# Kernel optimization log

Hardware: AMD Instinct MI355X
Metric: run time of the kernel (lower is better)

## Reference

```python
import jax, jax.numpy as jnp
import numpy as np

B, T, D, H = 4, 2048, 1024, 16
DK, DV, K, I = 48, 96, 4, 3072
EPS = 1e-5


def rmsnorm(x, w, eps=EPS):
    return x * jax.lax.rsqrt(jnp.mean(x * x, -1, keepdims=True) + eps) * w


def l2norm(x, eps=1e-6):
    return x * jax.lax.rsqrt(jnp.sum(x * x, -1, keepdims=True) + eps)


def causal_conv(x, w):
    # x: [B,T,C], w: [C,K]; causal depthwise conv (torch cross-correlation semantics)
    k = w.shape[1]
    xp = jnp.pad(x, ((0, 0), (k - 1, 0), (0, 0))).transpose(0, 2, 1)  # [B,C,T+K-1]
    y = jax.lax.conv_general_dilated(xp, w[:, None, :], (1,), 'VALID',
                                     feature_group_count=w.shape[0])
    return y.transpose(0, 2, 1)


def gated_delta_rule(q, k, v, g, beta):
    # q,k: [B,T,H,DK]  v: [B,T,H,DV]  g,beta: [B,T,H]
    scale = q.shape[-1] ** -0.5
    qT = jnp.moveaxis(q, 1, 0) * scale
    kT = jnp.moveaxis(k, 1, 0)
    vT = jnp.moveaxis(v, 1, 0)
    gT = jnp.moveaxis(g, 1, 0)
    bT = jnp.moveaxis(beta, 1, 0)
    S0 = jnp.zeros((q.shape[0], q.shape[2], q.shape[3], v.shape[3]), q.dtype)

    def step(S, inp):
        q_t, k_t, v_t, g_t, b_t = inp
        S = S * jnp.exp(g_t)[..., None, None]                      # gated decay
        v_new = (v_t - jnp.einsum('bhk,bhkv->bhv', k_t, S)) * b_t[..., None]
        S = S + k_t[..., None] * v_new[..., None, :]               # delta-rule update
        o_t = jnp.einsum('bhk,bhkv->bhv', q_t, S)
        return S, o_t

    _, o = jax.lax.scan(step, S0, (qT, kT, vT, gT, bT))
    return jnp.moveaxis(o, 0, 1)


def setup_inputs() -> dict:
    key = jax.random.key(0)
    ks = jax.random.split(key, 20)
    s = 0.02
    return {
        'hidden_states': jax.random.normal(ks[0], (B, T, D), jnp.float32),
        'norm1_w': jnp.ones((D,), jnp.float32),
        'q_w': jax.random.normal(ks[1], (D, H * DK), jnp.float32) * s,
        'k_w': jax.random.normal(ks[2], (D, H * DK), jnp.float32) * s,
        'v_w': jax.random.normal(ks[3], (D, H * DV), jnp.float32) * s,
        'conv_q_w': jax.random.normal(ks[4], (H * DK, K), jnp.float32) * 0.2,
        'conv_k_w': jax.random.normal(ks[5], (H * DK, K), jnp.float32) * 0.2,
        'conv_v_w': jax.random.normal(ks[6], (H * DV, K), jnp.float32) * 0.2,
        'b_w': jax.random.normal(ks[7], (D, H), jnp.float32) * s,
        'a_w': jax.random.normal(ks[8], (D, H), jnp.float32) * s,
        'A_log': jnp.log(jax.random.uniform(ks[9], (H,), jnp.float32, 1.0, 16.0)),
        'dt_bias': jax.random.normal(ks[10], (H,), jnp.float32) * 0.5,
        'g_w': jax.random.normal(ks[11], (D, H * DV), jnp.float32) * s,
        'o_norm_w': jnp.ones((DV,), jnp.float32),
        'o_w': jax.random.normal(ks[12], (H * DV, D), jnp.float32) * s,
        'norm2_w': jnp.ones((D,), jnp.float32),
        'gate_w': jax.random.normal(ks[13], (D, I), jnp.float32) * s,
        'up_w': jax.random.normal(ks[14], (D, I), jnp.float32) * s,
        'down_w': jax.random.normal(ks[15], (I, D), jnp.float32) * s,
    }


def reference(hidden_states, norm1_w, q_w, k_w, v_w, conv_q_w, conv_k_w, conv_v_w,
              b_w, a_w, A_log, dt_bias, g_w, o_norm_w, o_w, norm2_w,
              gate_w, up_w, down_w):
    x = hidden_states
    h = rmsnorm(x, norm1_w)
    # --- GatedDeltaNet mixer ---
    q = jax.nn.silu(causal_conv(h @ q_w, conv_q_w)).reshape(B, T, H, DK)
    k = jax.nn.silu(causal_conv(h @ k_w, conv_k_w)).reshape(B, T, H, DK)
    v = jax.nn.silu(causal_conv(h @ v_w, conv_v_w)).reshape(B, T, H, DV)
    q, k = l2norm(q), l2norm(k)
    beta = jax.nn.sigmoid(h @ b_w)                                  # [B,T,H]
    g = -jnp.exp(A_log) * jax.nn.softplus(h @ a_w + dt_bias)        # [B,T,H] mamba gate
    o = gated_delta_rule(q, k, v, g, beta)                          # [B,T,H,DV]
    gate = (h @ g_w).reshape(B, T, H, DV)
    o = rmsnorm(o, o_norm_w) * (gate * jax.nn.sigmoid(gate))        # fused gated RMSNorm
    x = x + o.reshape(B, T, H * DV) @ o_w
    # --- SwiGLU MLP ---
    h2 = rmsnorm(x, norm2_w)
    x = x + (jax.nn.silu(h2 @ gate_w) * (h2 @ up_w)) @ down_w
    return x
```

## Files before the change

kernel.cpp:

```cpp
#include <hip/hip_runtime.h>
#include <hip/hip_bf16.h>
#include <math.h>

constexpr int Bn = 4, Tn = 2048, Dn = 1024, Hn = 16, DKn = 48, DVn = 96, In = 3072;
constexpr int BT = Bn * Tn;
constexpr int HDK = Hn * DKn;
constexpr int HDV = Hn * DVn;
constexpr int QKVC = 2 * HDK + HDV;
constexpr int CC = 64;
constexpr int NC = Tn / CC;

using bf16 = __hip_bfloat16;
typedef __attribute__((ext_vector_type(8))) short bf16x8;
typedef __attribute__((ext_vector_type(4))) float f32x4;

constexpr size_t WO_HBF   = 0;
constexpr size_t WO_QKVR  = 16777216;
constexpr size_t WO_OSC   = 16777216;
constexpr size_t WO_ACT   = 16777216;
constexpr size_t WO_A     = 16777216;
constexpr size_t WO_B     = 26214400;
constexpr size_t WO_ST    = 45088768;
constexpr size_t WO_QKVC  = 67108864;
constexpr size_t WO_GATE  = 117440512;
constexpr size_t WO_X1    = 142606336;
constexpr size_t WO_BA    = 176160768;
constexpr size_t WO_GC    = 177209344;
constexpr size_t WO_T     = 177733632;
constexpr size_t WO_UV    = 194510848;
constexpr size_t WO_WB    = 219676672;
constexpr size_t WB_QKVT = 0;
constexpr size_t WB_GT   = 3145728;
constexpr size_t WB_OT   = 4718592;
constexpr size_t WB_GATET= 6291456;
constexpr size_t WB_UPT  = 9437184;
constexpr size_t WB_DOWNT= 12582912;
constexpr size_t WB_ABT  = 15728640;

__device__ __forceinline__ float sigmoidf_(float x) { return 1.f / (1.f + __expf(-x)); }
__device__ __forceinline__ float siluf(float x) { return x * sigmoidf_(x); }

__device__ __forceinline__ void glds16(const void* g, void* l) {
  __builtin_amdgcn_global_load_lds((const __attribute__((address_space(1))) void*)g,
                                   (__attribute__((address_space(3))) void*)l, 16, 0, 0);
}

__device__ __forceinline__ f32x4 mfma16(bf16x8 a, bf16x8 b, f32x4 c) {
  return __builtin_amdgcn_mfma_f32_16x16x32_bf16(a, b, c, 0, 0, 0);
}

__device__ __forceinline__ bf16x8 scale8(bf16x8 a, float s) {
  bf16x8 r;
#pragma unroll
  for (int e = 0; e < 8; e++) {
    float f = __bfloat162float(__ushort_as_bfloat16((unsigned short)a[e])) * s;
    r[e] = (short)__bfloat16_as_ushort(__float2bfloat16(f));
  }
  return r;
}

__device__ __forceinline__ float b2f(short u) {
  return __bfloat162float(__ushort_as_bfloat16((unsigned short)u));
}
__device__ __forceinline__ short f2b(float f) {
  return (short)__bfloat16_as_ushort(__float2bfloat16(f));
}

struct TcastArgs {
  const float* src[10];
  bf16* dst[10];
  int R[10], C[10], gxw[10], t0[10];
};

__global__ void tcast_all(TcastArgs a) {
  __shared__ float t[32][33];
  int bid = blockIdx.x;
  int i = 0;
#pragma unroll
  for (int k = 1; k < 10; k++) if (bid >= a.t0[k]) i = k;
  int lt = bid - a.t0[i];
  int gxw = a.gxw[i];
  int bx = lt % gxw, by = lt / gxw;
  const float* in = a.src[i];
  bf16* out = a.dst[i];
  int R = a.R[i], C = a.C[i];
  int tx = threadIdx.x, ty = threadIdx.y;
  int c0 = bx * 32, r0 = by * 32;
#pragma unroll
  for (int j = 0; j < 4; j++) {
    int r = ty + j * 8;
    float v = (c0 + tx < C) ? in[(size_t)(r0 + r) * C + c0 + tx] : 0.f;
    t[r][tx] = v;
  }
  __syncthreads();
#pragma unroll
  for (int j = 0; j < 4; j++) {
    int cc = ty + j * 8;
    if (c0 + cc < C) out[(size_t)(c0 + cc) * R + r0 + tx] = __float2bfloat16(t[tx][cc]);
  }
}

__global__ void rmsnorm_bf_k(const float* __restrict__ x, const float* __restrict__ w,
                             bf16* __restrict__ y) {
  int row = blockIdx.x;
  const float4* xr = (const float4*)(x + (size_t)row * Dn);
  int tid = threadIdx.x;
  float4 v = xr[tid];
  float ss = v.x * v.x + v.y * v.y + v.z * v.z + v.w * v.w;
  for (int m = 32; m >= 1; m >>= 1) ss += __shfl_xor(ss, m, 64);
  __shared__ float wsum[4];
  if ((tid & 63) == 0) wsum[tid >> 6] = ss;
  __syncthreads();
  ss = wsum[0] + wsum[1] + wsum[2] + wsum[3];
  float rs = rsqrtf(ss * (1.f / Dn) + 1e-5f);
  float4 wv = ((const float4*)w)[tid];
  bf16* yr = y + (size_t)row * Dn + tid * 4;
  yr[0] = __float2bfloat16(v.x * rs * wv.x);
  yr[1] = __float2bfloat16(v.y * rs * wv.y);
  yr[2] = __float2bfloat16(v.z * rs * wv.z);
  yr[3] = __float2bfloat16(v.w * rs * wv.w);
}

#define AS256(bi) (lds + (bi) * 8192)
#define BS256(bi) (lds + 32768 + (bi) * 8192)
#define STAGE256(bi, k0) do { \
    glds16(gA0 + (k0), AS256(bi) + w * 512); \
    glds16(gB0 + (k0), BS256(bi) + w * 512); \
  } while (0)

__global__ __launch_bounds__(1024) void gemm256(
    const bf16* __restrict__ A, const bf16* __restrict__ Bt,
    bf16* __restrict__ C0, bf16* __restrict__ C1,
    int gx, int N, int K, int mode) {
  __shared__ bf16 lds[65536];
  int nb = gx * 32;
  int q8 = nb >> 3;
  int bid = blockIdx.x;
  int sw = (bid & 7) * q8 + (bid >> 3);
  int by = sw & 31, bx = sw >> 5;
  int bm = by * 256, bn = bx * 256;
  int tid = threadIdx.x;
  int lane = tid & 63, w = tid >> 6;
  int l15 = lane & 15, lq = lane >> 4;
  int wr = w >> 2, wc = w & 3;
  int arow0 = tid >> 2;
  int srcq = (tid & 3) ^ ((arow0 >> 1) & 3);
  const bf16* gA0 = A + (size_t)(bm + arow0) * K + srcq * 8;
  const bf16* gB0 = Bt + (size_t)(bn + arow0) * K + srcq * 8;
  int slot = lq ^ ((l15 >> 1) & 3);
  f32x4 acc[4][4];
#pragma unroll
  for (int m = 0; m < 4; m++)
#pragma unroll
    for (int n = 0; n < 4; n++) acc[m][n] = (f32x4){0.f, 0.f, 0.f, 0.f};
  int NT = K >> 5;
  STAGE256(0, 0);
  STAGE256(1, 32);
  STAGE256(2, 64);
  for (int t = 0; t < NT; ++t) {
    int b = t & 3;
    if (t <= NT - 3)      { asm volatile("s_waitcnt vmcnt(4)" ::: "memory"); }
    else if (t == NT - 2) { asm volatile("s_waitcnt vmcnt(2)" ::: "memory"); }
    else                  { asm volatile("s_waitcnt vmcnt(0)" ::: "memory"); }
    __builtin_amdgcn_s_barrier();
    bf16x8 af[4], bfr[4];
#pragma unroll
    for (int m = 0; m < 4; m++)
      af[m] = *(const bf16x8*)(AS256(b) + (wr * 64 + m * 16 + l15) * 32 + slot * 8);
#pragma unroll
    for (int n = 0; n < 4; n++)
      bfr[n] = *(const bf16x8*)(BS256(b) + (wc * 64 + n * 16 + l15) * 32 + slot * 8);
    __builtin_amdgcn_s_setprio(1);
#pragma unroll
    for (int m = 0; m < 4; m++)
#pragma unroll
      for (int n = 0; n < 4; n++)
        acc[m][n] = mfma16(af[m], bfr[n], acc[m][n]);
    __builtin_amdgcn_s_setprio(0);
    if (t + 3 < NT) STAGE256((t + 3) & 3, (t + 3) * 32);
  }
  __syncthreads();
  bf16* dst; int ldc, bnl; bool doSilu;
  if (mode == 10) {
    if (bn < 3072) { dst = C0; ldc = 3072; bnl = bn; doSilu = false; }
    else           { dst = C1; ldc = 1536; bnl = bn - 3072; doSilu = false; }
  } else {
    if (bn < 3072) { dst = C0; ldc = 3072; bnl = bn; doSilu = true; }
    else           { dst = C1; ldc = 3072; bnl = bn - 3072; doSilu = false; }
  }
  bf16* cw = lds + w * 4096;
#pragma unroll
  for (int m = 0; m < 4; m++)
#pragma unroll
    for (int n = 0; n < 4; n++)
#pragma unroll
      for (int i = 0; i < 4; i++) {
        int row_l = m * 16 + lq * 4 + i;
        int col_l = n * 16 + l15;
        float v = acc[m][n][i];
        if (doSilu) v = siluf(v);
        cw[row_l * 64 + (col_l ^ ((row_l & 7) << 3))] = __float2bfloat16(v);
      }
  __syncthreads();
  int r8 = lane >> 3, cblk = lane & 7;
#pragma unroll
  for (int it = 0; it < 8; it++) {
    int row_l = it * 8 + r8;
    int sblk = cblk ^ (row_l & 7);
    bf16x8 val = *(const bf16x8*)&cw[row_l * 64 + sblk * 8];
    *(bf16x8*)&dst[(size_t)(bm + wr * 64 + row_l) * ldc + bnl + wc * 64 + cblk * 8] = val;
  }
}

__global__ __launch_bounds__(1024) void gemm_mfma(
    const bf16* __restrict__ A, const bf16* __restrict__ Bt,
    void* __restrict__ Cv, const float* __restrict__ res,
    int N, int K, int ldc, int mode) {
  __shared__ bf16 As[4][4096];
  __shared__ bf16 Bs[4][4096];
  int tid = threadIdx.x, lane = tid & 63, w = tid >> 6;
  int bm = blockIdx.y * 128, bn = blockIdx.x * 128;
  int l15 = lane & 15, lq = lane >> 4;
  int wr = w >> 2, wc = w & 3;
  int r0 = (tid & 511) >> 2;
  int sq = (tid & 3) ^ ((r0 >> 1) & 3);
  const bf16* g0;
  bf16* lb;
  if (w < 8) {
    g0 = A + (size_t)(bm + r0) * K + sq * 8;
    lb = &As[0][w * 512];
  } else {
    int br = bn + r0; if (br >= N) br = 0;
    g0 = Bt + (size_t)br * K + sq * 8;
    lb = &Bs[0][(w - 8) * 512];
  }
#define STAGE128X(bi, k0) glds16(g0 + (k0), lb + (bi) * 4096)
  int slot = lq ^ ((l15 >> 1) & 3);
  f32x4 acc[2][2];
#pragma unroll
  for (int m = 0; m < 2; m++)
#pragma unroll
    for (int n = 0; n < 2; n++) acc[m][n] = (f32x4){0.f, 0.f, 0.f, 0.f};
  int NT = K >> 5;
  STAGE128X(0, 0);
  STAGE128X(1, 32);
  STAGE128X(2, 64);
  for (int t = 0; t < NT; ++t) {
    int b = t & 3;
    if (t <= NT - 3)      { asm volatile("s_waitcnt vmcnt(2)" ::: "memory"); }
    else if (t == NT - 2) { asm volatile("s_waitcnt vmcnt(1)" ::: "memory"); }
    else                  { asm volatile("s_waitcnt vmcnt(0)" ::: "memory"); }
    __builtin_amdgcn_s_barrier();
    bf16x8 af[2], bfr[2];
#pragma unroll
    for (int m = 0; m < 2; m++)
      af[m] = *(const bf16x8*)&As[b][(wr * 32 + m * 16 + l15) * 32 + slot * 8];
#pragma unroll
    for (int n = 0; n < 2; n++)
      bfr[n] = *(const bf16x8*)&Bs[b][(wc * 32 + n * 16 + l15) * 32 + slot * 8];
    __builtin_amdgcn_s_setprio(1);
#pragma unroll
    for (int m = 0; m < 2; m++)
#pragma unroll
      for (int n = 0; n < 2; n++)
        acc[m][n] = mfma16(af[m], bfr[n], acc[m][n]);
    __builtin_amdgcn_s_setprio(0);
    if (t + 3 < NT) STAGE128X((t + 3) & 3, (t + 3) * 32);
  }
#pragma unroll
  for (int m = 0; m < 2; m++) {
#pragma unroll
    for (int n = 0; n < 2; n++) {
      int col = bn + wc * 32 + n * 16 + l15;
      if (col >= N) continue;
#pragma unroll
      for (int i = 0; i < 4; i++) {
        int row = bm + wr * 32 + m * 16 + lq * 4 + i;
        float v = acc[m][n][i];
        size_t idx = (size_t)row * ldc + col;
        if (mode == 0) {
          if (res) v += res[idx];
          ((float*)Cv)[idx] = v;
        } else {
          ((bf16*)Cv)[idx] = __float2bfloat16(v);
        }
      }
    }
  }
}

__global__ __launch_bounds__(256) void convsilu2_k(const bf16* __restrict__ in,
                                                   bf16* __restrict__ outp,
                                                   const float* __restrict__ wq,
                                                   const float* __restrict__ wk,
                                                   const float* __restrict__ wv) {
  int tx = threadIdx.x & 31;
  int ty = threadIdx.x >> 5;
  int c = (blockIdx.x * 32 + tx) * 8;
  int gt = blockIdx.y * 8 + ty;
  int b = gt >> 11, t = gt & (Tn - 1);
  const float* wsrc = (c < HDK) ? (wq + c * 4)
                     : (c < 2 * HDK) ? (wk + (c - HDK) * 4)
                                     : (wv + (c - 2 * HDK) * 4);
  float4 W[8];
#pragma unroll
  for (int j = 0; j < 8; j++) W[j] = ((const float4*)wsrc)[j];
  const bf16* base = in + (size_t)b * Tn * QKVC + c;
  bf16x8 r[4];
  bf16x8 zero = {0, 0, 0, 0, 0, 0, 0, 0};
#pragma unroll
  for (int j = 0; j < 4; j++) {
    int tt = t - 3 + j;
    r[j] = (tt >= 0) ? *(const bf16x8*)(base + (size_t)tt * QKVC) : zero;
  }
  bf16x8 o;
#pragma unroll
  for (int ch = 0; ch < 8; ch++) {
    float x0 = b2f(r[0][ch]), x1 = b2f(r[1][ch]), x2 = b2f(r[2][ch]), x3 = b2f(r[3][ch]);
    float y = x0 * W[ch].x + x1 * W[ch].y + x2 * W[ch].z + x3 * W[ch].w;
    o[ch] = f2b(siluf(y));
  }
  *(bf16x8*)(outp + (size_t)gt * QKVC + c) = o;
}

__global__ __launch_bounds__(256) void l2norm_k(bf16* __restrict__ qkv) {
  int row = blockIdx.x * 256 + threadIdx.x;
  int t = row >> 5, hr = row & 31;
  bf16* p = qkv + (size_t)t * QKVC + hr * DKn;
  bf16x8 v[6];
  float ss = 0.f;
#pragma unroll
  for (int j = 0; j < 6; j++) {
    v[j] = *(const bf16x8*)(p + j * 8);
#pragma unroll
    for (int e = 0; e < 8; e++) { float f = b2f(v[j][e]); ss += f * f; }
  }
  float rs = rsqrtf(ss + 1e-6f);
#pragma unroll
  for (int j = 0; j < 6; j++) {
    bf16x8 o;
#pragma unroll
    for (int e = 0; e < 8; e++) o[e] = f2b(b2f(v[j][e]) * rs);
    *(bf16x8*)(p + j * 8) = o;
  }
}

__global__ void betag_k(float* __restrict__ ba, const float* __restrict__ A_log,
                        const float* __restrict__ dt_bias) {
  int i = blockIdx.x * blockDim.x + threadIdx.x;
  int h = i & 15, r = i >> 4;
  float bv = ba[(size_t)r * 32 + h];
  float av = ba[(size_t)r * 32 + 16 + h];
  ba[(size_t)r * 32 + h] = sigmoidf_(bv);
  float xx = av + dt_bias[h];
  float sp = (xx > 20.f) ? xx : log1pf(__expf(xx));
  ba[(size_t)r * 32 + 16 + h] = -__expf(A_log[h]) * sp;
}

__global__ __launch_bounds__(256) void dn_p1a(const bf16* __restrict__ qkv,
                                              const float* __restrict__ ba,
                                              float* __restrict__ Gc_g,
                                              bf16* __restrict__ T_g,
                                              bf16* __restrict__ Uv_g,
                                              bf16* __restrict__ A_g,
                                              bf16* __restrict__ B_g) {
  __shared__ __align__(16) char smem[62976];
  bf16 (*Kl)[72]   = (bf16(*)[72])(smem);
  bf16 (*Tl)[72]   = (bf16(*)[72])(smem + 9216);
  bf16 (*UvdT)[72] = (bf16(*)[72])(smem + 18432);
  float* Gcl = (float*)(smem + 32256);
  float* Bl  = (float*)(smem + 32512);
  bf16 (*Vl)[100]  = (bf16(*)[100])(smem + 32768);
  float (*Nl)[68]  = (float(*)[68])(smem + 45568);
  bf16 (*KTl)[72]  = (bf16(*)[72])(smem + 32768);
  bf16 (*KTbl)[72] = (bf16(*)[72])(smem + 39680);
  bf16 (*M2T)[72]  = (bf16(*)[72])(smem + 46592);
  int cid = blockIdx.x;
  int nc = cid & (NC - 1);
  int bh = cid >> 5;
  int h = bh & 15, b = bh >> 4;
  int t0 = nc * CC;
  int tid = threadIdx.x, lane = tid & 63, w = tid >> 6;
  int l15 = lane & 15, qd = lane >> 4;
  bf16 zb = __float2bfloat16(0.f);
  {
    int t = tid >> 2, p = tid & 3;
    const bf16* row = qkv + ((size_t)(b * Tn + t0 + t)) * QKVC;
    int c0 = p * 12;
#pragma unroll
    for (int j = 0; j < 12; ++j) Kl[t][c0 + j] = row[HDK + h * DKn + c0 + j];
    int j0 = p * 24;
#pragma unroll
    for (int j = 0; j < 24; ++j) Vl[t][j0 + j] = row[2 * HDK + h * DVn + j0 + j];
  }
  for (int i = tid; i < 64 * 24; i += 256) {
    int t = i / 24, c = 48 + (i % 24);
    Kl[t][c] = zb;
  }
  if (tid < 64) {
    size_t row = (size_t)(b * Tn + t0 + tid);
    float g = ba[row * 32 + 16 + h];
    float be = ba[row * 32 + h];
    float acc = g;
#pragma unroll
    for (int d = 1; d < 64; d <<= 1) {
      float o = __shfl_up(acc, d);
      if (tid >= d) acc += o;
    }
    Gcl[tid] = acc; Bl[tid] = be;
    Gc_g[(size_t)bh * Tn + t0 + tid] = acc;
  }
  __syncthreads();
  f32x4 dacc[4];
#pragma unroll
  for (int n = 0; n < 4; n++) dacc[n] = (f32x4){0.f, 0.f, 0.f, 0.f};
  {
    int arow = w * 16 + l15;
    bf16x8 a0 = *(const bf16x8*)&Kl[arow][qd * 8];
    bf16x8 a1 = *(const bf16x8*)&Kl[arow][32 + qd * 8];
#pragma unroll
    for (int n = 0; n < 4; n++) {
      int brow = n * 16 + l15;
      bf16x8 b0 = *(const bf16x8*)&Kl[brow][qd * 8];
      bf16x8 b1 = *(const bf16x8*)&Kl[brow][32 + qd * 8];
      dacc[n] = mfma16(a0, b0, dacc[n]);
      dacc[n] = mfma16(a1, b1, dacc[n]);
    }
  }
#pragma unroll
  for (int i = 0; i < 4; i++) {
    int t = w * 16 + qd * 4 + i;
    float bt = Bl[t], gt = Gcl[t];
#pragma unroll
    for (int n = 0; n < 4; n++) {
      int s = n * 16 + l15;
      Nl[t][s] = (s < t) ? bt * __expf(gt - Gcl[s]) * dacc[n][i] : 0.f;
    }
  }
  __syncthreads();
  float g63 = Gcl[63];
  int c = tid;
  if (c < 160) {
    float R[64];
    if (c < 64) {
#pragma unroll
      for (int t = 0; t < 64; ++t) R[t] = (t == c) ? 1.f : 0.f;
    } else {
      int j = c - 64;
#pragma unroll
      for (int t = 0; t < 64; ++t) R[t] = Bl[t] * __bfloat162float(Vl[t][j]);
    }
#pragma unroll
    for (int t = 1; t < 64; ++t) {
      float a0 = 0.f, a1 = 0.f, a2 = 0.f, a3 = 0.f;
#pragma unroll
      for (int s = 0; s + 3 < t; s += 4) {
        float4 n4 = *(const float4*)&Nl[t][s];
        a0 += n4.x * R[s]; a1 += n4.y * R[s + 1];
        a2 += n4.z * R[s + 2]; a3 += n4.w * R[s + 3];
      }
#pragma unroll
      for (int s = t & ~3; s < t; ++s) a0 += Nl[t][s] * R[s];
      R[t] -= ((a0 + a1) + (a2 + a3));
    }
    if (c < 64) {
#pragma unroll
      for (int t = 0; t < 64; ++t) {
        bf16 v = __float2bfloat16(R[t]);
        T_g[(size_t)cid * 4096 + t * 64 + c] = v;
        Tl[t][c] = v;
      }
    } else {
      int j = c - 64;
#pragma unroll
      for (int t = 0; t < 64; ++t) {
        Uv_g[(size_t)cid * 6144 + t * 96 + j] = __float2bfloat16(R[t]);
        UvdT[j][t] = __float2bfloat16(R[t] * __expf(g63 - Gcl[t]));
      }
    }
  }
  __syncthreads();
  for (int i = tid; i < 48 * 64; i += 256) {
    int dk = i >> 6, t = i & 63;
    bf16 kv = Kl[t][dk];
    KTl[dk][t] = kv;
    float bl = Bl[t] * __expf(Gcl[t]);
    KTbl[dk][t] = __float2bfloat16(__bfloat162float(kv) * bl);
  }
  __syncthreads();
  f32x4 m1[3];
#pragma unroll
  for (int n = 0; n < 3; n++) m1[n] = (f32x4){0.f, 0.f, 0.f, 0.f};
  {
    int arow = w * 16 + l15;
    bf16x8 a0 = *(const bf16x8*)&Tl[arow][qd * 8];
    bf16x8 a1 = *(const bf16x8*)&Tl[arow][32 + qd * 8];
#pragma unroll
    for (int n = 0; n < 3; n++) {
      int brow = n * 16 + l15;
      bf16x8 b0 = *(const bf16x8*)&KTbl[brow][qd * 8];
      bf16x8 b1 = *(const bf16x8*)&KTbl[brow][32 + qd * 8];
      m1[n] = mfma16(a0, b0, m1[n]);
      m1[n] = mfma16(a1, b1, m1[n]);
    }
  }
#pragma unroll
  for (int i = 0; i < 4; i++) {
    int tt = w * 16 + qd * 4 + i;
    float dd = __expf(g63 - Gcl[tt]);
#pragma unroll
    for (int n = 0; n < 3; n++) {
      int dk = n * 16 + l15;
      M2T[dk][tt] = __float2bfloat16(m1[n][i] * dd);
    }
  }
  __syncthreads();
  float lamC = __expf(g63);
#pragma unroll
  for (int tswap = 0; tswap < 7; tswap++) {
    int t = w + 4 * tswap;
    if (t >= 27) break;
    int mi, ni; bool isA;
    if (t < 9) { isA = true; mi = t / 3; ni = t % 3; }
    else { isA = false; mi = (t - 9) / 6; ni = (t - 9) % 6; }
    f32x4 acc = (f32x4){0.f, 0.f, 0.f, 0.f};
    int arow = mi * 16 + l15;
    bf16x8 a0 = *(const bf16x8*)&KTl[arow][qd * 8];
    bf16x8 a1 = *(const bf16x8*)&KTl[arow][32 + qd * 8];
    int brow = ni * 16 + l15;
    if (isA) {
      bf16x8 b0 = *(const bf16x8*)&M2T[brow][qd * 8];
      bf16x8 b1 = *(const bf16x8*)&M2T[brow][32 + qd * 8];
      acc = mfma16(a0, b0, acc);
      acc = mfma16(a1, b1, acc);
#pragma unroll
      for (int i = 0; i < 4; i++) {
        int row = mi * 16 + qd * 4 + i, colv = ni * 16 + l15;
        float v = ((row == colv) ? lamC : 0.f) - acc[i];
        A_g[(size_t)cid * 2304 + row * 48 + colv] = __float2bfloat16(v);
      }
    } else {
      bf16x8 b0 = *(const bf16x8*)&UvdT[brow][qd * 8];
      bf16x8 b1 = *(const bf16x8*)&UvdT[brow][32 + qd * 8];
      acc = mfma16(a0, b0, acc);
      acc = mfma16(a1, b1, acc);
#pragma unroll
      for (int i = 0; i < 4; i++) {
        int row = mi * 16 + qd * 4 + i, colv = ni * 16 + l15;
        B_g[(size_t)cid * 4608 + row * 96 + colv] = __float2bfloat16(acc[i]);
      }
    }
  }
}

__global__ __launch_bounds__(256) void dn_p2b(const bf16* __restrict__ A_g,
                                              const bf16* __restrict__ B_g,
                                              bf16* __restrict__ St_g) {
  __shared__ bf16 STl[2][96][72];
  __shared__ bf16 Al[2][48][72];
  __shared__ bf16 Bl[2][4608];
  int bh = blockIdx.x;
  int tid = threadIdx.x, lane = tid & 63, w = tid >> 6;
  int l15 = lane & 15, qd = lane >> 4;
  bf16 zb = __float2bfloat16(0.f);
  for (int i = tid; i < 2 * 96 * 72; i += 256) (&STl[0][0][0])[i] = zb;
  for (int i = tid; i < 2 * 48 * 24; i += 256) {
    int buf = i / (48 * 24), r = (i / 24) % 48, cc = 48 + (i % 24);
    Al[buf][r][cc] = zb;
  }
  bf16x8 ra0, ra1, rb0, rb1;
  unsigned int rb2;
  int e_a0 = tid * 8, e_a1 = 2048 + tid * 8;
  {
    size_t cid = (size_t)bh * NC;
    ra0 = *(const bf16x8*)(A_g + cid * 2304 + e_a0);
    if (tid < 32) ra1 = *(const bf16x8*)(A_g + cid * 2304 + e_a1);
    rb0 = *(const bf16x8*)(B_g + cid * 4608 + tid * 16);
    rb1 = *(const bf16x8*)(B_g + cid * 4608 + tid * 16 + 8);
    rb2 = *(const unsigned int*)(B_g + cid * 4608 + 4096 + tid * 2);
  }
  *(bf16x8*)&Al[0][e_a0 / 48][e_a0 % 48] = ra0;
  if (tid < 32) *(bf16x8*)&Al[0][e_a1 / 48][e_a1 % 48] = ra1;
  *(bf16x8*)&Bl[0][tid * 16] = rb0;
  *(bf16x8*)&Bl[0][tid * 16 + 8] = rb1;
  *(unsigned int*)&Bl[0][4096 + tid * 2] = rb2;
  {
    size_t cid = (size_t)bh * NC + 1;
    ra0 = *(const bf16x8*)(A_g + cid * 2304 + e_a0);
    if (tid < 32) ra1 = *(const bf16x8*)(A_g + cid * 2304 + e_a1);
    rb0 = *(const bf16x8*)(B_g + cid * 4608 + tid * 16);
    rb1 = *(const bf16x8*)(B_g + cid * 4608 + tid * 16 + 8);
    rb2 = *(const unsigned int*)(B_g + cid * 4608 + 4096 + tid * 2);
  }
  __syncthreads();

  for (int c = 0; c < NC - 1; ++c) {
    int cur = c & 1, nxt = cur ^ 1;
    size_t cid = (size_t)bh * NC + c;
    {
      int e0 = tid * 8, e1 = 2048 + tid * 8, e2 = 4096 + tid * 2;
      *(bf16x8*)(St_g + cid * 4608 + e0) = *(const bf16x8*)&STl[cur][e0 / 48][e0 % 48];
      *(bf16x8*)(St_g + cid * 4608 + e1) = *(const bf16x8*)&STl[cur][e1 / 48][e1 % 48];
      *(unsigned int*)(St_g + cid * 4608 + e2) = *(const unsigned int*)&STl[cur][e2 / 48][e2 % 48];
    }
    float vals[5][4];
#pragma unroll
    for (int ts = 0; ts < 5; ts++) {
      int t = w + 4 * ts;
      if (t >= 18) break;
      int mi = t / 3, ni = t % 3;
      f32x4 acc = (f32x4){0.f, 0.f, 0.f, 0.f};
      int arow = mi * 16 + l15;
      bf16x8 a0 = *(const bf16x8*)&STl[cur][arow][qd * 8];
      bf16x8 a1 = *(const bf16x8*)&STl[cur][arow][32 + qd * 8];
      int brow = ni * 16 + l15;
      bf16x8 b0 = *(const bf16x8*)&Al[cur][brow][qd * 8];
      bf16x8 b1 = *(const bf16x8*)&Al[cur][brow][32 + qd * 8];
      acc = mfma16(a0, b0, acc);
      acc = mfma16(a1, b1, acc);
#pragma unroll
      for (int i = 0; i < 4; i++) {
        int dv = mi * 16 + qd * 4 + i, ii = ni * 16 + l15;
        vals[ts][i] = acc[i] + __bfloat162float(Bl[cur][ii * 96 + dv]);
      }
    }
#pragma unroll
    for (int ts = 0; ts < 5; ts++) {
      int t = w + 4 * ts;
      if (t >= 18) break;
      int mi = t / 3, ni = t % 3;
#pragma unroll
      for (int i = 0; i < 4; i++) {
        int dv = mi * 16 + qd * 4 + i, ii = ni * 16 + l15;
        STl[nxt][dv][ii] = __float2bfloat16(vals[ts][i]);
      }
    }
    if (c + 1 <= NC - 2) {
      *(bf16x8*)&Al[nxt][e_a0 / 48][e_a0 % 48] = ra0;
      if (tid < 32) *(bf16x8*)&Al[nxt][e_a1 / 48][e_a1 % 48] = ra1;
      *(bf16x8*)&Bl[nxt][tid * 16] = rb0;
      *(bf16x8*)&Bl[nxt][tid * 16 + 8] = rb1;
      *(unsigned int*)&Bl[nxt][4096 + tid * 2] = rb2;
      if (c + 2 <= NC - 2) {
        size_t cid2 = (size_t)bh * NC + c + 2;
        ra0 = *(const bf16x8*)(A_g + cid2 * 2304 + e_a0);
        if (tid < 32) ra1 = *(const bf16x8*)(A_g + cid2 * 2304 + e_a1);
        rb0 = *(const bf16x8*)(B_g + cid2 * 4608 + tid * 16);
        rb1 = *(const bf16x8*)(B_g + cid2 * 4608 + tid * 16 + 8);
        rb2 = *(const unsigned int*)(B_g + cid2 * 4608 + 4096 + tid * 2);
      }
    }
    __syncthreads();
  }
  {
    size_t cid = (size_t)bh * NC + (NC - 1);
    int cur = (NC - 1) & 1;
    int e0 = tid * 8, e1 = 2048 + tid * 8, e2 = 4096 + tid * 2;
    *(bf16x8*)(St_g + cid * 4608 + e0) = *(const bf16x8*)&STl[cur][e0 / 48][e0 % 48];
    *(bf16x8*)(St_g + cid * 4608 + e1) = *(const bf16x8*)&STl[cur][e1 / 48][e1 % 48];
    *(unsigned int*)(St_g + cid * 4608 + e2) = *(const unsigned int*)&STl[cur][e2 / 48][e2 % 48];
  }
}

__global__ __launch_bounds__(256) void dn_p2c(const bf16* __restrict__ qkv,
                                              const float* __restrict__ ba,
                                              const float* __restrict__ Gc_g,
                                              const bf16* __restrict__ T_g,
                                              const bf16* __restrict__ Uv_g,
                                              const bf16* __restrict__ St_g,
                                              const bf16* __restrict__ gate,
                                              const float* __restrict__ onw,
                                              bf16* __restrict__ attn) {
  __shared__ bf16 Kl[64][72], Ql[64][72], Tl[64][72], Ml[64][72];
  __shared__ bf16 G1T[96][72], UT[96][72], STb[96][72];
  __shared__ float Gcl[64], Bl[64];
  __shared__ float onwl[96];
  int cid = blockIdx.x;
  int nc = cid & (NC - 1);
  int bh = cid >> 5;
  int h = bh & 15, b = bh >> 4;
  int t0 = nc * CC;
  int tid = threadIdx.x, lane = tid & 63, w = tid >> 6;
  int l15 = lane & 15, qd = lane >> 4;
  const float scale = 0.14433756729740643f;
  bf16 zb = __float2bfloat16(0.f);
  {
    int t = tid >> 2, p = tid & 3;
    size_t grow = (size_t)(b * Tn + t0 + t);
    const bf16* row = qkv + grow * QKVC;
    int c0 = p * 12;
#pragma unroll
    for (int j = 0; j < 12; ++j) {
      int cc = c0 + j;
      Kl[t][cc] = row[HDK + h * DKn + cc];
      Ql[t][cc] = __float2bfloat16(__bfloat162float(row[h * DKn + cc]) * scale);
    }
    if (p == 0) { Gcl[t] = Gc_g[(size_t)bh * Tn + t0 + t]; Bl[t] = ba[grow * 32 + h]; }
  }
  if (tid < 96) onwl[tid] = onw[tid];
  for (int i = tid; i < 64 * 16; i += 256) {
    int t = i >> 4, cc = 48 + (i & 15);
    Kl[t][cc] = zb; Ql[t][cc] = zb;
  }
  for (int i = tid; i < 4096; i += 256)
    (&Tl[0][0])[(i >> 6) * 72 + (i & 63)] = T_g[(size_t)cid * 4096 + i];
  for (int i = tid; i < 4608; i += 256)
    STb[i / 48][i % 48] = St_g[(size_t)cid * 4608 + i];
  for (int i = tid; i < 96 * 16; i += 256)
    STb[i >> 4][48 + (i & 15)] = zb;
  __syncthreads();
  f32x4 acc[6];
#pragma unroll
  for (int n = 0; n < 6; n++) acc[n] = (f32x4){0.f, 0.f, 0.f, 0.f};
  {
    int arow = w * 16 + l15;
    bf16x8 a0 = *(const bf16x8*)&Kl[arow][qd * 8];
    bf16x8 a1 = *(const bf16x8*)&Kl[arow][32 + qd * 8];
#pragma unroll
    for (int n = 0; n < 6; n++) {
      int brow = n * 16 + l15;
      bf16x8 b0 = *(const bf16x8*)&STb[brow][qd * 8];
      bf16x8 b1 = *(const bf16x8*)&STb[brow][32 + qd * 8];
      acc[n] = mfma16(a0, b0, acc[n]);
      acc[n] = mfma16(a1, b1, acc[n]);
    }
  }
#pragma unroll
  for (int i = 0; i < 4; i++) {
    int tt = w * 16 + qd * 4 + i;
    float sc = Bl[tt] * __expf(Gcl[tt]);
#pragma unroll
    for (int n = 0; n < 6; n++)
      G1T[n * 16 + l15][tt] = __float2bfloat16(acc[n][i] * sc);
  }
  __syncthreads();
#pragma unroll
  for (int n = 0; n < 6; n++) acc[n] = (f32x4){0.f, 0.f, 0.f, 0.f};
  {
    int arow = w * 16 + l15;
    bf16x8 a0 = *(const bf16x8*)&Tl[arow][qd * 8];
    bf16x8 a1 = *(const bf16x8*)&Tl[arow][32 + qd * 8];
#pragma unroll
    for (int n = 0; n < 6; n++) {
      int brow = n * 16 + l15;
      bf16x8 b0 = *(const bf16x8*)&G1T[brow][qd * 8];
      bf16x8 b1 = *(const bf16x8*)&G1T[brow][32 + qd * 8];
      acc[n] = mfma16(a0, b0, acc[n]);
      acc[n] = mfma16(a1, b1, acc[n]);
    }
  }
#pragma unroll
  for (int i = 0; i < 4; i++) {
    int tt = w * 16 + qd * 4 + i;
#pragma unroll
    for (int n = 0; n < 6; n++) {
      int dv = n * 16 + l15;
      float uv = __bfloat162float(Uv_g[(size_t)cid * 6144 + tt * 96 + dv]);
      UT[dv][tt] = __float2bfloat16(uv - acc[n][i]);
    }
  }
  f32x4 qk[4];
#pragma unroll
  for (int n = 0; n < 4; n++) qk[n] = (f32x4){0.f, 0.f, 0.f, 0.f};
  {
    int arow = w * 16 + l15;
    bf16x8 a0 = *(const bf16x8*)&Ql[arow][qd * 8];
    bf16x8 a1 = *(const bf16x8*)&Ql[arow][32 + qd * 8];
#pragma unroll
    for (int n = 0; n < 4; n++) {
      int brow = n * 16 + l15;
      bf16x8 b0 = *(const bf16x8*)&Kl[brow][qd * 8];
      bf16x8 b1 = *(const bf16x8*)&Kl[brow][32 + qd * 8];
      qk[n] = mfma16(a0, b0, qk[n]);
      qk[n] = mfma16(a1, b1, qk[n]);
    }
  }
#pragma unroll
  for (int i = 0; i < 4; i++) {
    int tt = w * 16 + qd * 4 + i;
    float gt = Gcl[tt];
#pragma unroll
    for (int n = 0; n < 4; n++) {
      int ss = n * 16 + l15;
      float m = (ss <= tt) ? qk[n][i] * __expf(gt - Gcl[ss]) : 0.f;
      Ml[tt][ss] = __float2bfloat16(m);
    }
  }
  __syncthreads();
#pragma unroll
  for (int n = 0; n < 6; n++) acc[n] = (f32x4){0.f, 0.f, 0.f, 0.f};
  {
    int arow = w * 16 + l15;
    float lam = __expf(Gcl[arow]);
    bf16x8 a0 = scale8(*(const bf16x8*)&Ql[arow][qd * 8], lam);
    bf16x8 a1 = scale8(*(const bf16x8*)&Ql[arow][32 + qd * 8], lam);
    bf16x8 m0 = *(const bf16x8*)&Ml[arow][qd * 8];
    bf16x8 m1 = *(const bf16x8*)&Ml[arow][32 + qd * 8];
#pragma unroll
    for (int n = 0; n < 6; n++) {
      int brow = n * 16 + l15;
      bf16x8 b0 = *(const bf16x8*)&STb[brow][qd * 8];
      bf16x8 b1 = *(const bf16x8*)&STb[brow][32 + qd * 8];
      acc[n] = mfma16(a0, b0, acc[n]);
      acc[n] = mfma16(a1, b1, acc[n]);
      bf16x8 u0 = *(const bf16x8*)&UT[brow][qd * 8];
      bf16x8 u1 = *(const bf16x8*)&UT[brow][32 + qd * 8];
      acc[n] = mfma16(m0, u0, acc[n]);
      acc[n] = mfma16(m1, u1, acc[n]);
    }
  }
#pragma unroll
  for (int i = 0; i < 4; i++) {
    int tt = w * 16 + qd * 4 + i;
    float ss = 0.f;
#pragma unroll
    for (int n = 0; n < 6; n++) ss += acc[n][i] * acc[n][i];
    ss += __shfl_xor(ss, 1, 64);
    ss += __shfl_xor(ss, 2, 64);
    ss += __shfl_xor(ss, 4, 64);
    ss += __shfl_xor(ss, 8, 64);
    float rs = rsqrtf(ss * (1.f / DVn) + 1e-5f);
    size_t orow = ((size_t)(b * Tn + t0 + tt)) * HDV + h * DVn;
#pragma unroll
    for (int n = 0; n < 6; n++) {
      int dv = n * 16 + l15;
      float g = __bfloat162float(gate[orow + dv]);
      attn[orow + dv] = __float2bfloat16(acc[n][i] * rs * onwl[dv] * siluf(g));
    }
  }
}

__global__ __launch_bounds__(256) void silumul_bf_k(bf16* __restrict__ a,
                                                    const bf16* __restrict__ b) {
  size_t i = ((size_t)blockIdx.x * 256 + threadIdx.x) * 8;
  bf16x8 av = *(const bf16x8*)(a + i);
  bf16x8 bv = *(const bf16x8*)(b + i);
  bf16x8 r;
#pragma unroll
  for (int e = 0; e < 8; e++) r[e] = f2b(b2f(av[e]) * b2f(bv[e]));
  *(bf16x8*)(a + i) = r;
}

extern "C" void kernel_launch(void* const* d_in, const int* in_sizes, int n_in,
                              void* d_out, int out_size, void* d_ws, size_t ws_size,
                              hipStream_t stream) {
  const float* x       = (const float*)d_in[0];
  const float* norm1_w = (const float*)d_in[1];
  const float* q_w     = (const float*)d_in[2];
  const float* k_w     = (const float*)d_in[3];
  const float* v_w     = (const float*)d_in[4];
  const float* cq_w    = (const float*)d_in[5];
  const float* ck_w    = (const float*)d_in[6];
  const float* cv_w    = (const float*)d_in[7];
  const float* b_w     = (const float*)d_in[8];
  const float* a_w     = (const float*)d_in[9];
  const float* A_log   = (const float*)d_in[10];
  const float* dt_bias = (const float*)d_in[11];
  const float* g_w     = (const float*)d_in[12];
  const float* o_norm_w= (const float*)d_in[13];
  const float* o_w     = (const float*)d_in[14];
  const float* norm2_w = (const float*)d_in[15];
  const float* gate_w  = (const float*)d_in[16];
  const float* up_w    = (const float*)d_in[17];
  const float* down_w  = (const float*)d_in[18];
  char* wsb = (char*)d_ws;
  float* out = (float*)d_out;

  bf16*  hbf   = (bf16*)(wsb + WO_HBF);
  bf16*  qkvr  = (bf16*)(wsb + WO_QKVR);
  bf16*  qkvc  = (bf16*)(wsb + WO_QKVC);
  bf16*  upb   = (bf16*)(wsb + WO_QKVC);
  bf16*  attn  = (bf16*)(wsb + WO_OSC);
  bf16*  actb  = (bf16*)(wsb + WO_ACT);
  bf16*  gateb = (bf16*)(wsb + WO_GATE);
  float* x1    = (float*)(wsb + WO_X1);
  float* ba    = (float*)(wsb + WO_BA);
  float* Gc    = (float*)(wsb + WO_GC);
  bf16*  Tg    = (bf16*)(wsb + WO_T);
  bf16*  Uvg   = (bf16*)(wsb + WO_UV);
  bf16*  A_g   = (bf16*)(wsb + WO_A);
  bf16*  B_g   = (bf16*)(wsb + WO_B);
  bf16*  St_g  = (bf16*)(wsb + WO_ST);
  bf16*  wb    = (bf16*)(wsb + WO_WB);

  {
    TcastArgs ta;
    const float* srcs[10] = {q_w, k_w, v_w, g_w, o_w, gate_w, up_w, down_w, b_w, a_w};
    bf16* dsts[10] = {wb + WB_QKVT, wb + WB_QKVT + 768 * 1024, wb + WB_QKVT + 1536 * 1024,
                      wb + WB_GT, wb + WB_OT, wb + WB_GATET, wb + WB_UPT, wb + WB_DOWNT,
                      wb + WB_ABT, wb + WB_ABT + 16 * 1024};
    int Rs[10] = {1024, 1024, 1024, 1024, 1536, 1024, 1024, 3072, 1024, 1024};
    int Cs[10] = {768, 768, 1536, 1536, 1024, 3072, 3072, 1024, 16, 16};
    int off = 0;
    for (int i = 0; i < 10; i++) {
      ta.src[i] = srcs[i]; ta.dst[i] = dsts[i];
      ta.R[i] = Rs[i]; ta.C[i] = Cs[i];
      ta.gxw[i] = (Cs[i] + 31) / 32;
      ta.t0[i] = off;
      off += ta.gxw[i] * (Rs[i] / 32);
    }
    tcast_all<<<off, dim3(32, 8), 0, stream>>>(ta);
  }

  rmsnorm_bf_k<<<BT, 256, 0, stream>>>(x, norm1_w, hbf);
  gemm256<<<576, 1024, 0, stream>>>(hbf, wb + WB_QKVT, qkvr, gateb, 18, 4608, 1024, 10);
  gemm_mfma<<<dim3(1, 64), 1024, 0, stream>>>(hbf, wb + WB_ABT, ba, nullptr, 32, 1024, 32, 0);
  convsilu2_k<<<dim3(QKVC / 256, BT / 8), 256, 0, stream>>>(qkvr, qkvc, cq_w, ck_w, cv_w);
  l2norm_k<<<(BT * 32) / 256, 256, 0, stream>>>(qkvc);
  betag_k<<<(BT * Hn) / 256, 256, 0, stream>>>(ba, A_log, dt_bias);
  dn_p1a<<<Bn * Hn * NC, 256, 0, stream>>>(qkvc, ba, Gc, Tg, Uvg, A_g, B_g);
  dn_p2b<<<Bn * Hn, 256, 0, stream>>>(A_g, B_g, St_g);
  dn_p2c<<<Bn * Hn * NC, 256, 0, stream>>>(qkvc, ba, Gc, Tg, Uvg, St_g, gateb, o_norm_w, attn);
  gemm_mfma<<<dim3(8, 64), 1024, 0, stream>>>(attn, wb + WB_OT, x1, x, 1024, 1536, 1024, 0);
  rmsnorm_bf_k<<<BT, 256, 0, stream>>>(x1, norm2_w, hbf);
  gemm256<<<768, 1024, 0, stream>>>(hbf, wb + WB_GATET, actb, upb, 24, 6144, 1024, 11);
  silumul_bf_k<<<(BT * In) / (8 * 256), 256, 0, stream>>>(actb, upb);
  gemm_mfma<<<dim3(8, 64), 1024, 0, stream>>>(actb, wb + WB_DOWNT, out, x1, 1024, 3072, 1024, 0);
}
```

Baseline: 665.3 us.

## Fuse SwiGLU activation into gate/up GEMM epilogue via paired column tiles

Adds a dedicated MLP GEMM kernel where each block computes matching gate and up column tiles (128 columns each, offset by 3072 rows in the transposed weight) and applies silu(gate)*up in the epilogue. It writes only the activated product, removing the separate elementwise silu-multiply kernel and the write and re-read of the full gate and up intermediates. The old silu-mode path in gemm256 is dropped. Tile shape changes to 256x(128+128) with a swizzled block order, which changes per-wave accumulator layout and LDS use.

```diff
diff --git a/kernel.cpp b/kernel.cpp
--- a/kernel.cpp
+++ b/kernel.cpp
@@ -180,14 +180,9 @@
     if (t + 3 < NT) STAGE256((t + 3) & 3, (t + 3) * 32);
   }
   __syncthreads();
-  bf16* dst; int ldc, bnl; bool doSilu;
-  if (mode == 10) {
-    if (bn < 3072) { dst = C0; ldc = 3072; bnl = bn; doSilu = false; }
-    else           { dst = C1; ldc = 1536; bnl = bn - 3072; doSilu = false; }
-  } else {
-    if (bn < 3072) { dst = C0; ldc = 3072; bnl = bn; doSilu = true; }
-    else           { dst = C1; ldc = 3072; bnl = bn - 3072; doSilu = false; }
-  }
+  bf16* dst; int ldc, bnl;
+  if (bn < 3072) { dst = C0; ldc = 3072; bnl = bn; }
+  else           { dst = C1; ldc = 1536; bnl = bn - 3072; }
   bf16* cw = lds + w * 4096;
 #pragma unroll
   for (int m = 0; m < 4; m++)
@@ -197,9 +192,7 @@
       for (int i = 0; i < 4; i++) {
         int row_l = m * 16 + lq * 4 + i;
         int col_l = n * 16 + l15;
-        float v = acc[m][n][i];
-        if (doSilu) v = siluf(v);
-        cw[row_l * 64 + (col_l ^ ((row_l & 7) << 3))] = __float2bfloat16(v);
+        cw[row_l * 64 + (col_l ^ ((row_l & 7) << 3))] = __float2bfloat16(acc[m][n][i]);
       }
   __syncthreads();
   int r8 = lane >> 3, cblk = lane & 7;
@@ -209,6 +202,93 @@
     int sblk = cblk ^ (row_l & 7);
     bf16x8 val = *(const bf16x8*)&cw[row_l * 64 + sblk * 8];
     *(bf16x8*)&dst[(size_t)(bm + wr * 64 + row_l) * ldc + bnl + wc * 64 + cblk * 8] = val;
+  }
+}
+
+#define AMS(bi) (lds + (bi) * 8192)
+#define BMS(bi) (lds + 32768 + (bi) * 8192)
+#define STAGEML(bi, k0) do { \
+    glds16(gA0 + (k0), AMS(bi) + w * 512); \
+    glds16(gB0 + (k0), BMS(bi) + w * 512); \
+  } while (0)
+
+__global__ __launch_bounds__(1024) void gemm_mlp(
+    const bf16* __restrict__ A, const bf16* __restrict__ Bt,
+    bf16* __restrict__ C, int K) {
+  __shared__ bf16 lds[65536];
+  int bid = blockIdx.x;
+  int sw = (bid & 7) * 96 + (bid >> 3);
+  int by = sw & 31, bx = sw >> 5;
+  int bm = by * 256, bn = bx * 128;
+  int tid = threadIdx.x;
+  int lane = tid & 63, w = tid >> 6;
+  int l15 = lane & 15, lq = lane >> 4;
+  int wr = w >> 2, wc = w & 3;
+  int r0 = tid >> 2;
+  int srcq = (tid & 3) ^ ((r0 >> 1) & 3);
+  const bf16* gA0 = A + (size_t)(bm + r0) * K + srcq * 8;
+  int growB = bn + (r0 & 127) + (r0 >> 7) * 3072;
+  const bf16* gB0 = Bt + (size_t)growB * K + srcq * 8;
+  int slot = lq ^ ((l15 >> 1) & 3);
+  f32x4 accg[4][2], accu[4][2];
+#pragma unroll
+  for (int m = 0; m < 4; m++)
+#pragma unroll
+    for (int n = 0; n < 2; n++) {
+      accg[m][n] = (f32x4){0.f, 0.f, 0.f, 0.f};
+      accu[m][n] = (f32x4){0.f, 0.f, 0.f, 0.f};
+    }
+  int NT = K >> 5;
+  STAGEML(0, 0);
+  STAGEML(1, 32);
+  STAGEML(2, 64);
+  for (int t = 0; t < NT; ++t) {
+    int b = t & 3;
+    if (t <= NT - 3)      { asm volatile("s_waitcnt vmcnt(4)" ::: "memory"); }
+    else if (t == NT - 2) { asm volatile("s_waitcnt vmcnt(2)" ::: "memory"); }
+    else                  { asm volatile("s_waitcnt vmcnt(0)" ::: "memory"); }
+    __builtin_amdgcn_s_barrier();
+    bf16x8 af[4], bg[2], bu[2];
+#pragma unroll
+    for (int m = 0; m < 4; m++)
+      af[m] = *(const bf16x8*)(AMS(b) + (wr * 64 + m * 16 + l15) * 32 + slot * 8);
+#pragma unroll
+    for (int n = 0; n < 2; n++) {
+      bg[n] = *(const bf16x8*)(BMS(b) + (wc * 32 + n * 16 + l15) * 32 + slot * 8);
+      bu[n] = *(const bf16x8*)(BMS(b) + (128 + wc * 32 + n * 16 + l15) * 32 + slot * 8);
+    }
+    __builtin_amdgcn_s_setprio(1);
+#pragma unroll
+    for (int m = 0; m < 4; m++)
+#pragma unroll
+      for (int n = 0; n < 2; n++) {
+        accg[m][n] = mfma16(af[m], bg[n], accg[m][n]);
+        accu[m][n] = mfma16(af[m], bu[n], accu[m][n]);
+      }
+    __builtin_amdgcn_s_setprio(0);
+    if (t + 3 < NT) STAGEML((t + 3) & 3, (t + 3) * 32);
+  }
+  __syncthreads();
+  bf16* cw = lds + w * 2048;
+#pragma unroll
+  for (int m = 0; m < 4; m++)
+#pragma unroll
+    for (int n = 0; n < 2; n++)
+#pragma unroll
+      for (int i = 0; i < 4; i++) {
+        int row_l = m * 16 + lq * 4 + i;
+        int col_l = n * 16 + l15;
+        float v = siluf(accg[m][n][i]) * accu[m][n][i];
+        cw[row_l * 32 + (col_l ^ ((row_l & 3) << 3))] = __float2bfloat16(v);
+      }
+  __syncthreads();
+  int r16 = lane >> 2, cblk = lane & 3;
+#pragma unroll
+  for (int it = 0; it < 4; it++) {
+    int row_l = it * 16 + r16;
+    int sblk = cblk ^ (row_l & 3);
+    bf16x8 val = *(const bf16x8*)&cw[row_l * 32 + sblk * 8];
+    *(bf16x8*)&C[(size_t)(bm + wr * 64 + row_l) * 3072 + bn + wc * 32 + cblk * 8] = val;
   }
 }
 
@@ -830,17 +910,6 @@
   }
 }
 
-__global__ __launch_bounds__(256) void silumul_bf_k(bf16* __restrict__ a,
-                                                    const bf16* __restrict__ b) {
-  size_t i = ((size_t)blockIdx.x * 256 + threadIdx.x) * 8;
-  bf16x8 av = *(const bf16x8*)(a + i);
-  bf16x8 bv = *(const bf16x8*)(b + i);
-  bf16x8 r;
-#pragma unroll
-  for (int e = 0; e < 8; e++) r[e] = f2b(b2f(av[e]) * b2f(bv[e]));
-  *(bf16x8*)(a + i) = r;
-}
-
 extern "C" void kernel_launch(void* const* d_in, const int* in_sizes, int n_in,
                               void* d_out, int out_size, void* d_ws, size_t ws_size,
                               hipStream_t stream) {
@@ -869,7 +938,6 @@
   bf16*  hbf   = (bf16*)(wsb + WO_HBF);
   bf16*  qkvr  = (bf16*)(wsb + WO_QKVR);
   bf16*  qkvc  = (bf16*)(wsb + WO_QKVC);
-  bf16*  upb   = (bf16*)(wsb + WO_QKVC);
   bf16*  attn  = (bf16*)(wsb + WO_OSC);
   bf16*  actb  = (bf16*)(wsb + WO_ACT);
   bf16*  gateb = (bf16*)(wsb + WO_GATE);
@@ -913,7 +981,6 @@
   dn_p2c<<<Bn * Hn * NC, 256, 0, stream>>>(qkvc, ba, Gc, Tg, Uvg, St_g, gateb, o_norm_w, attn);
   gemm_mfma<<<dim3(8, 64), 1024, 0, stream>>>(attn, wb + WB_OT, x1, x, 1024, 1536, 1024, 0);
   rmsnorm_bf_k<<<BT, 256, 0, stream>>>(x1, norm2_w, hbf);
-  gemm256<<<768, 1024, 0, stream>>>(hbf, wb + WB_GATET, actb, upb, 24, 6144, 1024, 11);
-  silumul_bf_k<<<(BT * In) / (8 * 256), 256, 0, stream>>>(actb, upb);
+  gemm_mlp<<<768, 1024, 0, stream>>>(hbf, wb + WB_GATET, actb, 1024);
   gemm_mfma<<<dim3(8, 64), 1024, 0, stream>>>(actb, wb + WB_DOWNT, out, x1, 1024, 3072, 1024, 0);
 }
```

Result: faster. 616.1 us (-7.4%).
